# Optimization experiments

Measured on AMD Instinct MI355X. Metric: run time of the kernel, lower is better.

The kernel has to match this reference:

```python
import jax, jax.numpy as jnp
import numpy as np

B, L, D, N = 4, 4096, 1024, 1024  # d_state must equal d_model for the original broadcasting to work


def _bayes_linear(x, wmu, wlv, bmu, blv, key):
    """Reparameterized Bayesian linear: w = mu + exp(0.5*log_var)*eps."""
    kw, kb = jax.random.split(key)
    w = wmu + jnp.exp(0.5 * wlv) * jax.random.normal(kw, wmu.shape, wmu.dtype)
    b = bmu + jnp.exp(0.5 * blv) * jax.random.normal(kb, bmu.shape, bmu.dtype)
    return x @ w.T + b


def setup_inputs() -> dict:
    key = jax.random.key(0)
    ks = jax.random.split(key, 17)
    inp = {"x": jax.random.normal(ks[0], (B, L, D), jnp.float32)}
    shapes = {"A": (N, D), "Bp": (N, D), "C": (D, N), "dt": (N, D)}
    i = 1
    for name, (o, ii) in shapes.items():
        # torch init: mu ~ N(0, 0.1), log_var ~ N(-9, 0.1)
        inp[f"{name}_wmu"] = 0.1 * jax.random.normal(ks[i], (o, ii), jnp.float32); i += 1
        inp[f"{name}_wlv"] = -9.0 + 0.1 * jax.random.normal(ks[i], (o, ii), jnp.float32); i += 1
        inp[f"{name}_bmu"] = 0.1 * jax.random.normal(ks[i], (o,), jnp.float32); i += 1
        inp[f"{name}_blv"] = -9.0 + 0.1 * jax.random.normal(ks[i], (o,), jnp.float32); i += 1
    return inp


def reference(x, A_wmu, A_wlv, A_bmu, A_blv,
              Bp_wmu, Bp_wlv, Bp_bmu, Bp_blv,
              C_wmu, C_wlv, C_bmu, C_blv,
              dt_wmu, dt_wlv, dt_bmu, dt_blv):
    key = jax.random.key(42)
    kA, kB, kC, kdt = jax.random.split(key, 4)
    A = -jnp.exp(_bayes_linear(x, A_wmu, A_wlv, A_bmu, A_blv, kA))   # [B,L,N]
    dt = jnp.exp(_bayes_linear(x, dt_wmu, dt_wlv, dt_bmu, dt_blv, kdt))
    Bm = _bayes_linear(x, Bp_wmu, Bp_wlv, Bp_bmu, Bp_blv, kB)        # [B,L,N]
    C = _bayes_linear(x, C_wmu, C_wlv, C_bmu, C_blv, kC)             # [B,L,D]

    E = jnp.exp(A * dt)   # per-step decay, [B,L,N]
    Bx = Bm * x           # input injection (requires N == D, as in original)

    def step(h, inp):
        e, bx, c = inp
        h = h * e + bx
        return h, c * h

    ET = jnp.swapaxes(E, 0, 1)    # time-major [L,B,N]
    BxT = jnp.swapaxes(Bx, 0, 1)
    CT = jnp.swapaxes(C, 0, 1)
    h0 = jnp.zeros((x.shape[0], N), x.dtype)
    _, yT = jax.lax.scan(step, h0, (ET, BxT, CT))
    # The torch code broadcasts h to [B,B,N] and sums over dim=1; h is identical
    # along that axis, so the sum equals multiplying by batch_size.
    return jnp.swapaxes(yT, 0, 1) * x.shape[0]
```

## Files before the change

kernel.cpp:

```cpp
#include <hip/hip_runtime.h>
#include <cstdint>

__host__ __device__ inline void tf2x32(uint32_t k0, uint32_t k1,
                                       uint32_t x0, uint32_t x1,
                                       uint32_t& o0, uint32_t& o1) {
  uint32_t ks2 = k0 ^ k1 ^ 0x1BD11BDAu;
  uint32_t v0 = x0 + k0, v1 = x1 + k1;
#define TFR(r) { v0 += v1; v1 = (v1 << r) | (v1 >> (32 - r)); v1 ^= v0; }
  TFR(13) TFR(15) TFR(26) TFR(6)
  v0 += k1;  v1 += ks2 + 1u;
  TFR(17) TFR(29) TFR(16) TFR(24)
  v0 += ks2; v1 += k0 + 2u;
  TFR(13) TFR(15) TFR(26) TFR(6)
  v0 += k0;  v1 += k1 + 3u;
  TFR(17) TFR(29) TFR(16) TFR(24)
  v0 += k1;  v1 += ks2 + 4u;
  TFR(13) TFR(15) TFR(26) TFR(6)
  v0 += ks2; v1 += k0 + 5u;
#undef TFR
  o0 = v0; o1 = v1;
}

__device__ inline float erfinv32(float x) {
  float w = -log1pf(-x * x);
  float p;
  if (w < 5.0f) {
    w -= 2.5f;
    p = 2.81022636e-08f;
    p = fmaf(p, w, 3.43273939e-07f);
    p = fmaf(p, w, -3.5233877e-06f);
    p = fmaf(p, w, -4.39150654e-06f);
    p = fmaf(p, w, 0.00021858087f);
    p = fmaf(p, w, -0.00125372503f);
    p = fmaf(p, w, -0.00417768164f);
    p = fmaf(p, w, 0.246640727f);
    p = fmaf(p, w, 1.50140941f);
  } else {
    w = sqrtf(w) - 3.0f;
    p = -0.000200214257f;
    p = fmaf(p, w, 0.000100950558f);
    p = fmaf(p, w, 0.00134934322f);
    p = fmaf(p, w, -0.00367342844f);
    p = fmaf(p, w, 0.00573950773f);
    p = fmaf(p, w, -0.0076224613f);
    p = fmaf(p, w, 0.00943887047f);
    p = fmaf(p, w, 1.00167406f);
    p = fmaf(p, w, 2.83297682f);
  }
  return p * x;
}

__device__ inline float rng_normal(uint32_t k0, uint32_t k1, uint32_t idx) {
  uint32_t o0, o1;
  tf2x32(k0, k1, 0u, idx, o0, o1);
  uint32_t bits = o0 ^ o1;
  float f = __uint_as_float((bits >> 9) | 0x3f800000u) - 1.0f;
  const float lo = -0.999999940395355224609375f;
  float u = fmaxf(lo, f * 2.0f + lo);
  return 1.41421356237f * erfinv32(u);
}

struct RngKeys {
  uint32_t wA0, wA1, bA0, bA1;
  uint32_t wB0, wB1, bB0, bB1;
  uint32_t wC0, wC1, bC0, bC1;
  uint32_t wD0, wD1, bD0, bD1;
};

typedef _Float16 f16x8 __attribute__((ext_vector_type(8)));
typedef _Float16 f16x4 __attribute__((ext_vector_type(4)));
typedef float f32x4 __attribute__((ext_vector_type(4)));

__global__ __launch_bounds__(256) void gen_weights(
    const float* __restrict__ Awmu, const float* __restrict__ Awlv,
    const float* __restrict__ Dwmu, const float* __restrict__ Dwlv,
    const float* __restrict__ Bwmu, const float* __restrict__ Bwlv,
    const float* __restrict__ Cwmu, const float* __restrict__ Cwlv,
    _Float16* __restrict__ Wh, RngKeys kk) {
  uint32_t idx = blockIdx.x * 256u + threadIdx.x;
  uint32_t sel = idx >> 20;
  uint32_t e = idx & 0xFFFFFu;
  float w;
  if (sel == 0u) {
    w = Awmu[e] + expf(0.5f * Awlv[e]) * rng_normal(kk.wA0, kk.wA1, e)
      + Dwmu[e] + expf(0.5f * Dwlv[e]) * rng_normal(kk.wD0, kk.wD1, e);
  } else if (sel == 1u) {
    w = Bwmu[e] + expf(0.5f * Bwlv[e]) * rng_normal(kk.wB0, kk.wB1, e);
  } else {
    w = Cwmu[e] + expf(0.5f * Cwlv[e]) * rng_normal(kk.wC0, kk.wC1, e);
  }
  Wh[idx] = (_Float16)w;
}

__global__ __launch_bounds__(256) void gen_bias(
    const float* __restrict__ Abmu, const float* __restrict__ Ablv,
    const float* __restrict__ Dbmu, const float* __restrict__ Dblv,
    const float* __restrict__ Bbmu, const float* __restrict__ Bblv,
    const float* __restrict__ Cbmu, const float* __restrict__ Cblv,
    float* __restrict__ bcat, RngKeys kk) {
  uint32_t o = blockIdx.x * 256u + threadIdx.x;
  uint32_t e = o & 1023u;
  float b;
  if (o < 1024u)
    b = Abmu[e] + expf(0.5f * Ablv[e]) * rng_normal(kk.bA0, kk.bA1, e)
      + Dbmu[e] + expf(0.5f * Dblv[e]) * rng_normal(kk.bD0, kk.bD1, e);
  else if (o < 2048u)
    b = Bbmu[e] + expf(0.5f * Bblv[e]) * rng_normal(kk.bB0, kk.bB1, e);
  else
    b = Cbmu[e] + expf(0.5f * Cblv[e]) * rng_normal(kk.bC0, kk.bC1, e);
  bcat[o] = b;
}

__global__ __launch_bounds__(256) void convert_x(const float* __restrict__ X,
                                                 _Float16* __restrict__ Xh) {
  size_t i4 = ((size_t)blockIdx.x * 256 + threadIdx.x) * 4;
  float4 v = *(const float4*)(X + i4);
  f16x4 h;
  h[0] = (_Float16)v.x; h[1] = (_Float16)v.y;
  h[2] = (_Float16)v.z; h[3] = (_Float16)v.w;
  *(f16x4*)(Xh + i4) = h;
}

__device__ inline void gl2lds16(const void* g, void* l) {
  __builtin_amdgcn_global_load_lds(
      (const __attribute__((address_space(1))) void*)g,
      (__attribute__((address_space(3))) void*)l, 16, 0, 0);
}

#define STAGE_A(BUF, KT, H)                                            \
  do {                                                                 \
    const _Float16* g_ = gA0 + (size_t)((H) * 128) * 1024 + (KT) * 64; \
    char* l_ = (char*)(&sA[(BUF)][(H)][0]) + tid * 16;                 \
    gl2lds16(g_, l_);                                                  \
    gl2lds16(g_ + 64 * 1024, l_ + 8192);                               \
  } while (0)

#define STAGE_B(BUF, KT, H)                                            \
  do {                                                                 \
    const _Float16* g_ = gB0 + (size_t)((H) * 128) * 1024 + (KT) * 64; \
    char* l_ = (char*)(&sB[(BUF)][(H)][0]) + tid * 16;                 \
    gl2lds16(g_, l_);                                                  \
    gl2lds16(g_ + 64 * 1024, l_ + 8192);                               \
  } while (0)

#define READ_A(CUR, MH)                                                \
  do {                                                                 \
    _Pragma("unroll") for (int k_ = 0; k_ < 4; ++k_) {                 \
      const int ro_ = abase + k_ * 1024;                               \
      ah[2 * k_]     = *(const f16x8*)&sA[(CUR)][(MH)][ro_ + so0];     \
      ah[2 * k_ + 1] = *(const f16x8*)&sA[(CUR)][(MH)][ro_ + so1];     \
    }                                                                  \
  } while (0)

#define READ_B(CUR, NH)                                                \
  do {                                                                 \
    _Pragma("unroll") for (int j_ = 0; j_ < 2; ++j_) {                 \
      const int ro_ = bbase + j_ * 1024;                               \
      bh[2 * j_]     = *(const f16x8*)&sB[(CUR)][(NH)][ro_ + so0];     \
      bh[2 * j_ + 1] = *(const f16x8*)&sB[(CUR)][(NH)][ro_ + so1];     \
    }                                                                  \
  } while (0)

#define QUAD(MH, NH)                                                         \
  do {                                                                       \
    _Pragma("unroll") for (int k_ = 0; k_ < 4; ++k_)                         \
      _Pragma("unroll") for (int j_ = 0; j_ < 2; ++j_) {                     \
        f32x4 c_ = acc[(MH) * 4 + k_][(NH) * 2 + j_];                        \
        c_ = __builtin_amdgcn_mfma_f32_16x16x32_f16(ah[2 * k_], bh[2 * j_],  \
                                                    c_, 0, 0, 0);            \
        c_ = __builtin_amdgcn_mfma_f32_16x16x32_f16(                         \
            ah[2 * k_ + 1], bh[2 * j_ + 1], c_, 0, 0, 0);                    \
        acc[(MH) * 4 + k_][(NH) * 2 + j_] = c_;                              \
      }                                                                      \
  } while (0)

#define VMW(N) asm volatile("s_waitcnt vmcnt(" #N ")" ::: "memory")
#define MFMA_PRE()                                       \
  do {                                                   \
    asm volatile("s_waitcnt lgkmcnt(0)" ::: "memory");   \
    __builtin_amdgcn_sched_barrier(0);                   \
    __builtin_amdgcn_s_setprio(1);                       \
  } while (0)
#define MFMA_POST()                                      \
  do {                                                   \
    __builtin_amdgcn_s_setprio(0);                       \
    __builtin_amdgcn_s_barrier();                        \
  } while (0)

__global__ __launch_bounds__(512, 2) void gemm_fused(
    const _Float16* __restrict__ Xh, const _Float16* __restrict__ Wh,
    const float* __restrict__ X, const float* __restrict__ bcat,
    _Float16* __restrict__ Z, float* __restrict__ out) {
  __shared__ _Float16 sA[2][2][128 * 64];
  __shared__ _Float16 sB[2][2][128 * 64];

  const int tid = threadIdx.x;

  const int swz = ((int)blockIdx.x & 7) * 96 + ((int)blockIdx.x >> 3);
  const int mt = swz / 12;
  const int nt = swz - mt * 12;
  const int m0 = mt * 256;
  const int n0 = nt * 256;

  const int srow = tid >> 3;
  const int sc = (tid & 7) ^ (srow & 7);
  const _Float16* gA0 = Xh + (size_t)(m0 + srow) * 1024 + sc * 8;
  const _Float16* gB0 = Wh + (size_t)(n0 + srow) * 1024 + sc * 8;

  const int lane = tid & 63;
  const int wave = tid >> 6;
  const int wm = wave >> 2;
  const int wn = wave & 3;
  const int fr = lane & 15;
  const int q = lane >> 4;
  const int f7 = fr & 7;
  const int so0 = (q ^ f7) * 8;
  const int so1 = so0 ^ 32;

  const int abase = (wm * 64 + fr) * 64;
  const int bbase = (wn * 32 + fr) * 64;

  f32x4 acc[8][4] = {};
  f16x8 ah[8], bh[4];

  STAGE_A(0, 0, 0);
  STAGE_B(0, 0, 0);
  STAGE_B(0, 0, 1);
  STAGE_A(0, 0, 1);
  VMW(4);
  __builtin_amdgcn_s_barrier();

  for (int kt = 0; kt < 15; ++kt) {
    const int cur = kt & 1;
    const int nxt = cur ^ 1;
    READ_A(cur, 0);
    READ_B(cur, 0);
    STAGE_A(nxt, kt + 1, 0);
    VMW(4);
    __builtin_amdgcn_s_barrier();
    MFMA_PRE(); QUAD(0, 0); MFMA_POST();
    READ_B(cur, 1);
    STAGE_B(nxt, kt + 1, 0);
    VMW(4);
    __builtin_amdgcn_s_barrier();
    MFMA_PRE(); QUAD(0, 1); MFMA_POST();
    READ_A(cur, 1);
    STAGE_B(nxt, kt + 1, 1);
    __builtin_amdgcn_s_barrier();
    MFMA_PRE(); QUAD(1, 1); MFMA_POST();
    READ_B(cur, 0);
    STAGE_A(nxt, kt + 1, 1);
    VMW(4);
    __builtin_amdgcn_s_barrier();
    MFMA_PRE(); QUAD(1, 0); MFMA_POST();
  }
  READ_A(1, 0);
  READ_B(1, 0);
  VMW(2);
  __builtin_amdgcn_s_barrier();
  MFMA_PRE(); QUAD(0, 0); MFMA_POST();
  READ_B(1, 1);
  VMW(0);
  __builtin_amdgcn_s_barrier();
  MFMA_PRE(); QUAD(0, 1); MFMA_POST();
  READ_A(1, 1);
  MFMA_PRE(); QUAD(1, 1);
  __builtin_amdgcn_s_setprio(0);
  READ_B(1, 0);
  MFMA_PRE(); QUAD(1, 0);
  __builtin_amdgcn_s_setprio(0);
  __builtin_amdgcn_sched_barrier(0);

  const int seg = n0 >> 10;
  const int mrow = (lane >> 4) * 4;
#pragma unroll
  for (int nfg = 0; nfg < 4; ++nfg) {
    const int nh = nfg >> 1, j = nfg & 1;
    const int n = n0 + wn * 32 + nh * 128 + j * 16 + fr;
    const float bv = bcat[n];
#pragma unroll
    for (int mf = 0; mf < 8; ++mf) {
      const int mh = mf >> 2, k = mf & 3;
      const int mbase = m0 + wm * 64 + mh * 128 + k * 16 + mrow;
      f32x4 a = acc[mf][nfg];
#pragma unroll
      for (int r = 0; r < 4; ++r) {
        const int m = mbase + r;
        const float v = a[r] + bv;
        if (seg == 0) {
          Z[(size_t)m * 2048 + n] = (_Float16)expf(-expf(v));
        } else if (seg == 1) {
          Z[(size_t)m * 2048 + n] =
              (_Float16)(v * X[(size_t)m * 1024 + (n - 1024)]);
        } else {
          out[(size_t)m * 1024 + (n - 2048)] = v;
        }
      }
    }
  }
}

#define LSEQ 4096
#define NC 64
#define LC 64
#define ZW 2048

__global__ __launch_bounds__(256) void scan_chunk(const _Float16* __restrict__ Z,
                                                  float* __restrict__ ac,
                                                  float* __restrict__ uc) {
  int n4 = threadIdx.x * 4;
  int c = blockIdx.y;
  int b = blockIdx.z;
  const _Float16* base = Z + (size_t)(b * LSEQ + c * LC) * ZW;
  float a[4] = {1.0f, 1.0f, 1.0f, 1.0f};
  float u[4] = {0.0f, 0.0f, 0.0f, 0.0f};
#pragma unroll 4
  for (int l = 0; l < LC; ++l) {
    f16x4 ev = *(const f16x4*)&base[(size_t)l * ZW + n4];
    f16x4 bx = *(const f16x4*)&base[(size_t)l * ZW + 1024 + n4];
#pragma unroll
    for (int i = 0; i < 4; ++i) {
      float e = (float)ev[i];
      a[i] *= e;
      u[i] = fmaf(e, u[i], (float)bx[i]);
    }
  }
  size_t o = ((size_t)b * NC + c) * 1024 + n4;
  *(float4*)&ac[o] = make_float4(a[0], a[1], a[2], a[3]);
  *(float4*)&uc[o] = make_float4(u[0], u[1], u[2], u[3]);
}

__global__ __launch_bounds__(256) void scan_prefix(const float* __restrict__ ac,
                                                   const float* __restrict__ uc,
                                                   float* __restrict__ hin) {
  int idx = blockIdx.x * 256 + threadIdx.x;
  int b = idx >> 10, n = idx & 1023;
  float h = 0.0f;
  for (int c = 0; c < NC; ++c) {
    size_t o = ((size_t)b * NC + c) * 1024 + n;
    hin[o] = h;
    h = fmaf(ac[o], h, uc[o]);
  }
}

__global__ __launch_bounds__(256) void scan_final(const _Float16* __restrict__ Z,
                                                  const float* __restrict__ hin,
                                                  float* __restrict__ out) {
  int n4 = threadIdx.x * 4;
  int c = blockIdx.y;
  int b = blockIdx.z;
  const _Float16* base = Z + (size_t)(b * LSEQ + c * LC) * ZW;
  float* obase = out + (size_t)(b * LSEQ + c * LC) * 1024;
  size_t ho = ((size_t)b * NC + c) * 1024 + n4;
  float4 hv = *(const float4*)&hin[ho];
  float h[4] = {hv.x, hv.y, hv.z, hv.w};
#pragma unroll 4
  for (int l = 0; l < LC; ++l) {
    f16x4 ev = *(const f16x4*)&base[(size_t)l * ZW + n4];
    f16x4 bx = *(const f16x4*)&base[(size_t)l * ZW + 1024 + n4];
    float4 cc = *(const float4*)&obase[(size_t)l * 1024 + n4];
#pragma unroll
    for (int i = 0; i < 4; ++i)
      h[i] = fmaf((float)ev[i], h[i], (float)bx[i]);
    *(float4*)&obase[(size_t)l * 1024 + n4] =
        make_float4(cc.x * h[0] * 4.0f, cc.y * h[1] * 4.0f,
                    cc.z * h[2] * 4.0f, cc.w * h[3] * 4.0f);
  }
}

extern "C" void kernel_launch(void* const* d_in, const int* in_sizes, int n_in,
                              void* d_out, int out_size, void* d_ws, size_t ws_size,
                              hipStream_t stream) {
  const float* x    = (const float*)d_in[0];
  const float* Awmu = (const float*)d_in[1];
  const float* Awlv = (const float*)d_in[2];
  const float* Abmu = (const float*)d_in[3];
  const float* Ablv = (const float*)d_in[4];
  const float* Bwmu = (const float*)d_in[5];
  const float* Bwlv = (const float*)d_in[6];
  const float* Bbmu = (const float*)d_in[7];
  const float* Bblv = (const float*)d_in[8];
  const float* Cwmu = (const float*)d_in[9];
  const float* Cwlv = (const float*)d_in[10];
  const float* Cbmu = (const float*)d_in[11];
  const float* Cblv = (const float*)d_in[12];
  const float* Dwmu = (const float*)d_in[13];
  const float* Dwlv = (const float*)d_in[14];
  const float* Dbmu = (const float*)d_in[15];
  const float* Dblv = (const float*)d_in[16];

  uint32_t k4[4][2];
  for (uint32_t i = 0; i < 4; ++i)
    tf2x32(0u, 42u, 0u, i, k4[i][0], k4[i][1]);
  RngKeys kk;
  tf2x32(k4[0][0], k4[0][1], 0u, 0u, kk.wA0, kk.wA1);
  tf2x32(k4[0][0], k4[0][1], 0u, 1u, kk.bA0, kk.bA1);
  tf2x32(k4[1][0], k4[1][1], 0u, 0u, kk.wB0, kk.wB1);
  tf2x32(k4[1][0], k4[1][1], 0u, 1u, kk.bB0, kk.bB1);
  tf2x32(k4[2][0], k4[2][1], 0u, 0u, kk.wC0, kk.wC1);
  tf2x32(k4[2][0], k4[2][1], 0u, 1u, kk.bC0, kk.bC1);
  tf2x32(k4[3][0], k4[3][1], 0u, 0u, kk.wD0, kk.wD1);
  tf2x32(k4[3][0], k4[3][1], 0u, 1u, kk.bD0, kk.bD1);

  char* ws = (char*)d_ws;
  const size_t OFF_WH   = 0;
  const size_t OFF_BCAT = 6291456;
  const size_t OFF_XH   = 8388608;
  const size_t OFF_Z    = 41943040;
  const size_t OFF_AC   = OFF_Z + (size_t)16384 * 2048 * 2;
  const size_t OFF_UC   = OFF_AC + (size_t)4 * NC * 1024 * 4;
  const size_t OFF_HIN  = OFF_UC + (size_t)4 * NC * 1024 * 4;
  const size_t NEEDED   = OFF_HIN + (size_t)4 * NC * 1024 * 4;
  if (ws_size < NEEDED) return;

  _Float16* Wh  = (_Float16*)(ws + OFF_WH);
  float*    bcat= (float*)(ws + OFF_BCAT);
  _Float16* Xh  = (_Float16*)(ws + OFF_XH);
  _Float16* Z   = (_Float16*)(ws + OFF_Z);
  float*    ac  = (float*)(ws + OFF_AC);
  float*    ucv = (float*)(ws + OFF_UC);
  float*    hin = (float*)(ws + OFF_HIN);
  float*    out = (float*)d_out;

  gen_weights<<<dim3(12288), dim3(256), 0, stream>>>(
      Awmu, Awlv, Dwmu, Dwlv, Bwmu, Bwlv, Cwmu, Cwlv, Wh, kk);
  gen_bias<<<dim3(12), dim3(256), 0, stream>>>(
      Abmu, Ablv, Dbmu, Dblv, Bbmu, Bblv, Cbmu, Cblv, bcat, kk);
  convert_x<<<dim3(16384), dim3(256), 0, stream>>>(x, Xh);
  gemm_fused<<<dim3(768), dim3(512), 0, stream>>>(
      Xh, Wh, x, bcat, Z, out);
  scan_chunk<<<dim3(1, NC, 4), dim3(256), 0, stream>>>(Z, ac, ucv);
  scan_prefix<<<dim3(16), dim3(256), 0, stream>>>(ac, ucv, hin);
  scan_final<<<dim3(1, NC, 4), dim3(256), 0, stream>>>(Z, hin, out);
}
```

Measured before the change: 406.5 us.

## Double-buffer LDS fragment registers to overlap ds_reads with MFMA quadrants

Splits the A and B register fragments into two sets each (ahE/ahO, bh0/bh1), so the next quadrant's LDS reads are issued before the current quadrant's MFMAs and waited on with partial lgkmcnt counts instead of lgkmcnt(0). The first A/B fragments of the next k-tile are prefetched at the end of each iteration. The aim is to hide LDS read latency behind matrix math. The cost is higher VGPR pressure at 512 threads with 2 blocks per CU, which could cause spills, and the barrier placement is more delicate.

```diff
diff --git a/kernel.cpp b/kernel.cpp
--- a/kernel.cpp
+++ b/kernel.cpp
@@ -143,49 +143,46 @@
     gl2lds16(g_ + 64 * 1024, l_ + 8192);                               \
   } while (0)
 
-#define READ_A(CUR, MH)                                                \
+#define RD_A(DST, CUR, MH)                                             \
   do {                                                                 \
     _Pragma("unroll") for (int k_ = 0; k_ < 4; ++k_) {                 \
       const int ro_ = abase + k_ * 1024;                               \
-      ah[2 * k_]     = *(const f16x8*)&sA[(CUR)][(MH)][ro_ + so0];     \
-      ah[2 * k_ + 1] = *(const f16x8*)&sA[(CUR)][(MH)][ro_ + so1];     \
+      DST[2 * k_]     = *(const f16x8*)&sA[(CUR)][(MH)][ro_ + so0];    \
+      DST[2 * k_ + 1] = *(const f16x8*)&sA[(CUR)][(MH)][ro_ + so1];    \
     }                                                                  \
   } while (0)
 
-#define READ_B(CUR, NH)                                                \
+#define RD_B(DST, CUR, NH)                                             \
   do {                                                                 \
     _Pragma("unroll") for (int j_ = 0; j_ < 2; ++j_) {                 \
       const int ro_ = bbase + j_ * 1024;                               \
-      bh[2 * j_]     = *(const f16x8*)&sB[(CUR)][(NH)][ro_ + so0];     \
-      bh[2 * j_ + 1] = *(const f16x8*)&sB[(CUR)][(NH)][ro_ + so1];     \
+      DST[2 * j_]     = *(const f16x8*)&sB[(CUR)][(NH)][ro_ + so0];    \
+      DST[2 * j_ + 1] = *(const f16x8*)&sB[(CUR)][(NH)][ro_ + so1];    \
     }                                                                  \
   } while (0)
 
-#define QUAD(MH, NH)                                                         \
+#define QUADX(AR, BR, MH, NH)                                                \
   do {                                                                       \
     _Pragma("unroll") for (int k_ = 0; k_ < 4; ++k_)                         \
       _Pragma("unroll") for (int j_ = 0; j_ < 2; ++j_) {                     \
         f32x4 c_ = acc[(MH) * 4 + k_][(NH) * 2 + j_];                        \
-        c_ = __builtin_amdgcn_mfma_f32_16x16x32_f16(ah[2 * k_], bh[2 * j_],  \
+        c_ = __builtin_amdgcn_mfma_f32_16x16x32_f16(AR[2 * k_], BR[2 * j_],  \
                                                     c_, 0, 0, 0);            \
         c_ = __builtin_amdgcn_mfma_f32_16x16x32_f16(                         \
-            ah[2 * k_ + 1], bh[2 * j_ + 1], c_, 0, 0, 0);                    \
+            AR[2 * k_ + 1], BR[2 * j_ + 1], c_, 0, 0, 0);                    \
         acc[(MH) * 4 + k_][(NH) * 2 + j_] = c_;                              \
       }                                                                      \
   } while (0)
 
 #define VMW(N) asm volatile("s_waitcnt vmcnt(" #N ")" ::: "memory")
-#define MFMA_PRE()                                       \
-  do {                                                   \
-    asm volatile("s_waitcnt lgkmcnt(0)" ::: "memory");   \
-    __builtin_amdgcn_sched_barrier(0);                   \
-    __builtin_amdgcn_s_setprio(1);                       \
-  } while (0)
-#define MFMA_POST()                                      \
-  do {                                                   \
-    __builtin_amdgcn_s_setprio(0);                       \
-    __builtin_amdgcn_s_barrier();                        \
-  } while (0)
+#define LGKM(N)                                                \
+  do {                                                         \
+    asm volatile("s_waitcnt lgkmcnt(" #N ")" ::: "memory");    \
+    __builtin_amdgcn_sched_barrier(0);                         \
+  } while (0)
+#define BAR() __builtin_amdgcn_s_barrier()
+#define PRIO1() __builtin_amdgcn_s_setprio(1)
+#define PRIO0() __builtin_amdgcn_s_setprio(0)
 
 __global__ __launch_bounds__(512, 2) void gemm_fused(
     const _Float16* __restrict__ Xh, const _Float16* __restrict__ Wh,
@@ -221,54 +218,66 @@
   const int bbase = (wn * 32 + fr) * 64;
 
   f32x4 acc[8][4] = {};
-  f16x8 ah[8], bh[4];
+  f16x8 ahE[8], ahO[8], bh0[4], bh1[4];
 
   STAGE_A(0, 0, 0);
   STAGE_B(0, 0, 0);
   STAGE_B(0, 0, 1);
   STAGE_A(0, 0, 1);
   VMW(4);
-  __builtin_amdgcn_s_barrier();
+  BAR();
+  RD_A(ahE, 0, 0);
+  RD_B(bh0, 0, 0);
 
   for (int kt = 0; kt < 15; ++kt) {
     const int cur = kt & 1;
     const int nxt = cur ^ 1;
-    READ_A(cur, 0);
-    READ_B(cur, 0);
     STAGE_A(nxt, kt + 1, 0);
     VMW(4);
-    __builtin_amdgcn_s_barrier();
-    MFMA_PRE(); QUAD(0, 0); MFMA_POST();
-    READ_B(cur, 1);
+    BAR();
+    RD_B(bh1, cur, 1);
+    LGKM(4);
+    PRIO1(); QUADX(ahE, bh0, 0, 0); PRIO0();
+    BAR();
     STAGE_B(nxt, kt + 1, 0);
     VMW(4);
-    __builtin_amdgcn_s_barrier();
-    MFMA_PRE(); QUAD(0, 1); MFMA_POST();
-    READ_A(cur, 1);
+    BAR();
+    RD_A(ahO, cur, 1);
+    LGKM(8);
+    PRIO1(); QUADX(ahE, bh1, 0, 1); PRIO0();
+    BAR();
     STAGE_B(nxt, kt + 1, 1);
-    __builtin_amdgcn_s_barrier();
-    MFMA_PRE(); QUAD(1, 1); MFMA_POST();
-    READ_B(cur, 0);
+    BAR();
+    RD_B(bh0, cur, 0);
+    LGKM(4);
+    PRIO1(); QUADX(ahO, bh1, 1, 1); PRIO0();
+    BAR();
     STAGE_A(nxt, kt + 1, 1);
     VMW(4);
-    __builtin_amdgcn_s_barrier();
-    MFMA_PRE(); QUAD(1, 0); MFMA_POST();
-  }
-  READ_A(1, 0);
-  READ_B(1, 0);
+    BAR();
+    LGKM(0);
+    PRIO1(); QUADX(ahO, bh0, 1, 0); PRIO0();
+    RD_A(ahE, nxt, 0);
+    RD_B(bh0, nxt, 0);
+    BAR();
+  }
   VMW(2);
-  __builtin_amdgcn_s_barrier();
-  MFMA_PRE(); QUAD(0, 0); MFMA_POST();
-  READ_B(1, 1);
+  BAR();
+  RD_B(bh1, 1, 1);
+  LGKM(4);
+  PRIO1(); QUADX(ahE, bh0, 0, 0); PRIO0();
+  BAR();
   VMW(0);
-  __builtin_amdgcn_s_barrier();
-  MFMA_PRE(); QUAD(0, 1); MFMA_POST();
-  READ_A(1, 1);
-  MFMA_PRE(); QUAD(1, 1);
-  __builtin_amdgcn_s_setprio(0);
-  READ_B(1, 0);
-  MFMA_PRE(); QUAD(1, 0);
-  __builtin_amdgcn_s_setprio(0);
+  BAR();
+  RD_A(ahO, 1, 1);
+  LGKM(8);
+  PRIO1(); QUADX(ahE, bh1, 0, 1); PRIO0();
+  BAR();
+  RD_B(bh0, 1, 0);
+  LGKM(4);
+  PRIO1(); QUADX(ahO, bh1, 1, 1); PRIO0();
+  LGKM(0);
+  PRIO1(); QUADX(ahO, bh0, 1, 0); PRIO0();
   __builtin_amdgcn_sched_barrier(0);
 
   const int seg = n0 >> 10;
```

Measured after the change: 416.4 us. 2.4% more time.
